# Optimization experiments

Measured on AMD Instinct MI355X. Metric: run time of the kernel, lower is better.

Reference implementation:

```python
import jax, jax.numpy as jnp
import numpy as np

DIM = 768
NUM_HEADS = 12
HEAD_DIM = DIM // NUM_HEADS
SCALE = HEAD_DIM ** -0.5


def setup_inputs() -> dict:
    key = jax.random.key(0)
    ks = jax.random.split(key, 7)
    B, N, C = 8, 1024, DIM
    x = jax.random.normal(ks[0], (B, N, C), dtype=jnp.float32)
    mask = jax.random.randint(ks[1], (B, N), 0, 2) > 0  # True = masked out
    qkv_w = jax.random.normal(ks[2], (3 * C, C), dtype=jnp.float32) * 0.02
    q_bias = jax.random.normal(ks[3], (C,), dtype=jnp.float32) * 0.02
    v_bias = jax.random.normal(ks[4], (C,), dtype=jnp.float32) * 0.02
    proj_w = jax.random.normal(ks[5], (C, C), dtype=jnp.float32) * 0.02
    proj_b = jax.random.normal(ks[6], (C,), dtype=jnp.float32) * 0.02
    return {"x": x, "mask": mask, "qkv_w": qkv_w, "q_bias": q_bias,
            "v_bias": v_bias, "proj_w": proj_w, "proj_b": proj_b}


def reference(x, mask, qkv_w, q_bias, v_bias, proj_w, proj_b):
    B, N, C = x.shape
    # CAE bias: concat(q_bias, zeros, v_bias) for the fused qkv projection
    qkv_bias = jnp.concatenate([q_bias, jnp.zeros_like(v_bias), v_bias])
    qkv = x @ qkv_w.T + qkv_bias  # [B, N, 3C]
    qkv = qkv.reshape(B, N, 3, NUM_HEADS, HEAD_DIM)
    q, k, v = (qkv[:, :, i].transpose(0, 2, 1, 3) for i in range(3))  # [B,H,N,hd]
    attn = jnp.einsum('bhqd,bhkd->bhqk', q * SCALE, k)  # [B,H,N,N]
    attn = jnp.where(mask[:, None, None, :], -jnp.inf, attn)
    attn = jax.nn.softmax(attn, axis=-1)
    out = jnp.einsum('bhqk,bhkd->bhqd', attn, v)  # [B,H,N,hd]
    out = out.transpose(0, 2, 1, 3).reshape(B, N, C)
    return out @ proj_w.T + proj_b
```

## Files before the change

### kernel.cpp

```cpp
#include <hip/hip_runtime.h>
#include <cstddef>
#include <cstdint>


typedef __attribute__((ext_vector_type(4))) float f32x4;
typedef __attribute__((ext_vector_type(8))) __bf16 bf16x8;
typedef __attribute__((ext_vector_type(4))) unsigned int uint4v;
typedef __attribute__((ext_vector_type(2))) unsigned int uint2v;

#define QK_PRESCALE 0.18033688011112042f

__device__ __forceinline__ unsigned short f2bf(float f) {
  return (unsigned short)((__float_as_uint(f) + 0x8000u) >> 16);
}
__device__ __forceinline__ unsigned int pack2bf(float flo, float fhi) {
  unsigned ulo = __float_as_uint(flo) + 0x8000u;
  unsigned uhi = __float_as_uint(fhi) + 0x8000u;
  return __builtin_amdgcn_perm(uhi, ulo, 0x07060302);
}

__device__ __forceinline__ void gl_lds16(const unsigned short* g, unsigned short* l) {
  __builtin_amdgcn_global_load_lds(
      (const __attribute__((address_space(1))) unsigned int*)g,
      (__attribute__((address_space(3))) unsigned int*)l, 16, 0, 0);
}

__global__ __launch_bounds__(256)
void cvt3_kernel(const float* __restrict__ s0, unsigned short* __restrict__ d0,
                 const float* __restrict__ s1, unsigned short* __restrict__ d1,
                 const float* __restrict__ s2, unsigned short* __restrict__ d2) {
  int bid = blockIdx.x;
  const float* s; unsigned short* d; int i; int n4;
  if (bid < 6144)      { s = s0; d = d0; i = bid * 256 + threadIdx.x;            n4 = 1572864; }
  else if (bid < 7872) { s = s1; d = d1; i = (bid - 6144) * 256 + threadIdx.x;   n4 = 442368; }
  else                 { s = s2; d = d2; i = (bid - 7872) * 256 + threadIdx.x;   n4 = 147456; }
  if (i < n4) {
    float4 v = ((const float4*)s)[i];
    uint2v o;
    o.x = pack2bf(v.x, v.y);
    o.y = pack2bf(v.z, v.w);
    ((uint2v*)d)[i] = o;
  }
}

__device__ __forceinline__ int a0row(int o) { return (o < 10) ? o * 8 : 144 + (o - 10) * 8; }
__device__ __forceinline__ int a1row(int o) { return (o < 8) ? 80 + o * 8 : 224 + (o - 8) * 8; }

__global__ __launch_bounds__(512, 2)
void qkv_gemm(const unsigned short* __restrict__ xb, const unsigned short* __restrict__ wb,
              const float* __restrict__ qb, const float* __restrict__ vb,
              unsigned short* __restrict__ qo, unsigned short* __restrict__ ko,
              unsigned short* __restrict__ vto) {
  __shared__ __align__(16) unsigned short lds[69632];
  const int tid = threadIdx.x;
  const int lane = tid & 63, wid = tid >> 6;
  const int widu = __builtin_amdgcn_readfirstlane(wid);
  const int lm = lane & 15, lq = lane >> 4;
  const int xsw = lm & 7;
  const int wr = widu >> 2, wc = widu & 3;
  const int L = blockIdx.x;
  const int xcd = L & 7, s = L >> 3;
  const int tt = xcd * 4 + (s >> 3);
  const int ft = s & 7;
  const int m0 = tt * 256;
  const int n0 = ft * 288;
  const int srow = lane >> 3;
  const int scolsw = ((lane & 7) ^ srow) * 8;
  const unsigned short* paS = wb + (size_t)(n0 + srow) * 768 + scolsw;
  const unsigned short* pbS = xb + (size_t)(m0 + srow) * 768 + scolsw;

  const int a0n3 = (widu < 4);
  const int a0o = a0n3 ? widu * 3 : 12 + (widu - 4) * 2;
  const int a0r0 = a0row(a0o), a0r1 = a0row(a0o + 1);
  const int a0r2 = a0n3 ? a0row(a0o + 2) : 0;
  const int a1r0 = a1row(2 * widu), a1r1 = a1row(2 * widu + 1);
  const int b0q0 = (2 * widu) >> 2, b0q1 = (2 * widu + 1) >> 2;
  const int b0r0 = b0q0 * 64 + ((2 * widu) & 3) * 8;
  const int b0r1 = b0q1 * 64 + ((2 * widu + 1) & 3) * 8;
  const int b1r0 = b0r0 + 32, b1r1 = b0r1 + 32;

  f32x4 acc[9][4] = {};

#define STAGE_A0(tgt) { const size_t _c = (size_t)(tgt) * 64; const int _b = ((tgt) & 1) * 18432; \
    gl_lds16(paS + (size_t)a0r0 * 768 + _c, &lds[_b + a0r0 * 64]); \
    gl_lds16(paS + (size_t)a0r1 * 768 + _c, &lds[_b + a0r1 * 64]); \
    if (a0n3) gl_lds16(paS + (size_t)a0r2 * 768 + _c, &lds[_b + a0r2 * 64]); }

#define STAGE_A1(tgt) { const size_t _c = (size_t)(tgt) * 64; const int _b = ((tgt) & 1) * 18432; \
    gl_lds16(paS + (size_t)a1r0 * 768 + _c, &lds[_b + a1r0 * 64]); \
    gl_lds16(paS + (size_t)a1r1 * 768 + _c, &lds[_b + a1r1 * 64]); }

#define STAGE_B0(tgt) { const size_t _c = (size_t)(tgt) * 64; const int _b = 36864 + ((tgt) & 1) * 16384; \
    gl_lds16(pbS + (size_t)b0r0 * 768 + _c, &lds[_b + b0r0 * 64]); \
    gl_lds16(pbS + (size_t)b0r1 * 768 + _c, &lds[_b + b0r1 * 64]); }

#define STAGE_B1(tgt) { const size_t _c = (size_t)(tgt) * 64; const int _b = 36864 + ((tgt) & 1) * 16384; \
    gl_lds16(pbS + (size_t)b1r0 * 768 + _c, &lds[_b + b1r0 * 64]); \
    gl_lds16(pbS + (size_t)b1r1 * 768 + _c, &lds[_b + b1r1 * 64]); }

#define WAIT_G() { if (a0n3) asm volatile("s_waitcnt vmcnt(5)" ::: "memory"); \
                   else      asm volatile("s_waitcnt vmcnt(4)" ::: "memory"); \
                   asm volatile("s_barrier" ::: "memory"); }
#define BAR_E()   asm volatile("s_waitcnt lgkmcnt(0)\ns_barrier" ::: "memory")

  STAGE_A0(0); STAGE_B0(0); STAGE_A1(0); STAGE_B1(0);
  STAGE_A0(1); STAGE_B0(1);
  WAIT_G();

  for (int t = 0; t < 12; ++t) {
    const int b = t & 1;
    const int tn1 = (t + 1 < 12) ? t + 1 : 11;
    const int tn2 = (t + 2 < 12) ? t + 2 : 11;
    const unsigned short* Ab = &lds[b * 18432];
    const unsigned short* Bb = &lds[36864 + b * 16384];

    bf16x8 bff[4][2], af[5][2];
#pragma unroll
    for (int n2 = 0; n2 < 4; ++n2)
#pragma unroll
      for (int kx = 0; kx < 2; ++kx)
        bff[n2][kx] = *(const bf16x8*)&Bb[(wc * 64 + n2 * 16 + lm) * 64 + (((kx * 4 + lq) ^ xsw) * 8)];
#pragma unroll
    for (int m2 = 0; m2 < 5; ++m2)
#pragma unroll
      for (int kx = 0; kx < 2; ++kx)
        af[m2][kx] = *(const bf16x8*)&Ab[(wr * 144 + m2 * 16 + lm) * 64 + (((kx * 4 + lq) ^ xsw) * 8)];

    STAGE_A1(tn1); STAGE_B1(tn1);

    __builtin_amdgcn_s_setprio(1);
#pragma unroll
    for (int kx = 0; kx < 2; ++kx)
#pragma unroll
      for (int m2 = 0; m2 < 5; ++m2)
#pragma unroll
        for (int n2 = 0; n2 < 4; ++n2)
          acc[m2][n2] = __builtin_amdgcn_mfma_f32_16x16x32_bf16(af[m2][kx], bff[n2][kx], acc[m2][n2], 0, 0, 0);
    __builtin_amdgcn_s_setprio(0);

    bf16x8 af2[4][2];
#pragma unroll
    for (int m2 = 0; m2 < 4; ++m2)
#pragma unroll
      for (int kx = 0; kx < 2; ++kx)
        af2[m2][kx] = *(const bf16x8*)&Ab[(wr * 144 + (5 + m2) * 16 + lm) * 64 + (((kx * 4 + lq) ^ xsw) * 8)];
    __builtin_amdgcn_s_setprio(1);
#pragma unroll
    for (int kx = 0; kx < 2; ++kx)
#pragma unroll
      for (int m2 = 0; m2 < 4; ++m2)
#pragma unroll
        for (int n2 = 0; n2 < 4; ++n2)
          acc[5 + m2][n2] = __builtin_amdgcn_mfma_f32_16x16x32_bf16(af2[m2][kx], bff[n2][kx], acc[5 + m2][n2], 0, 0, 0);
    __builtin_amdgcn_s_setprio(0);

    BAR_E();
    STAGE_A0(tn2); STAGE_B0(tn2);
    WAIT_G();
  }
  asm volatile("s_waitcnt vmcnt(0)" ::: "memory");

#undef STAGE_A0
#undef STAGE_A1
#undef STAGE_B0
#undef STAGE_B1

  const int bq = tt >> 2;
  const int tokb = (tt & 3) * 256;
#pragma unroll
  for (int mi = 0; mi < 9; ++mi) {
    const int fblk = n0 + wr * 144 + mi * 16;
    if (fblk < 1536) {
      const bool isq = fblk < 768;
      unsigned short* dst0 = isq ? qo : ko;
      const int fd = fblk - (isq ? 0 : 768);
      const int hh = fd >> 6;
      const int dih = (fd & 63) + lq * 4;
      f32x4 bias4 = {0.f, 0.f, 0.f, 0.f};
      if (isq) bias4 = *(const f32x4*)&qb[fblk + lq * 4];
#pragma unroll
      for (int ni = 0; ni < 4; ++ni) {
        const int tok = tokb + wc * 64 + ni * 16 + lm;
        uint2v pk;
        if (isq) {
          pk.x = pack2bf((acc[mi][ni][0] + bias4[0]) * QK_PRESCALE,
                         (acc[mi][ni][1] + bias4[1]) * QK_PRESCALE);
          pk.y = pack2bf((acc[mi][ni][2] + bias4[2]) * QK_PRESCALE,
                         (acc[mi][ni][3] + bias4[3]) * QK_PRESCALE);
        } else {
          pk.x = pack2bf(acc[mi][ni][0], acc[mi][ni][1]);
          pk.y = pack2bf(acc[mi][ni][2], acc[mi][ni][3]);
        }
        *(uint2v*)&dst0[(((size_t)(bq * 12 + hh)) * 1024 + tok) * 64 + dih] = pk;
      }
    }
  }
  if (n0 + 288 > 1536) {
#pragma unroll
    for (int p = 0; p < 2; ++p) {
      __syncthreads();
      if (wr == p) {
#pragma unroll
        for (int mi = 0; mi < 9; ++mi) {
          const int fblk = n0 + p * 144 + mi * 16;
          if (fblk >= 1536) {
            f32x4 bias4 = *(const f32x4*)&vb[fblk - 1536 + lq * 4];
#pragma unroll
            for (int ni = 0; ni < 4; ++ni) {
              const int tokl = wc * 64 + ni * 16 + lm;
#pragma unroll
              for (int r = 0; r < 4; ++r)
                lds[(mi * 16 + lq * 4 + r) * 264 + tokl] = f2bf(acc[mi][ni][r] + bias4[r]);
            }
          }
        }
      }
      __syncthreads();
      const int fv = 1536 - (n0 + p * 144);
      const int rv0 = fv > 0 ? fv : 0;
      for (int r = rv0 + (tid >> 2); r < 144; r += 128) {
        const int tq = tid & 3;
        const int dgv = n0 + p * 144 + r - 1536;
        const int hh = dgv >> 6, d = dgv & 63;
        unsigned short* dstv = vto + (((size_t)(bq * 12 + hh)) * 64 + d) * 1024 + tokb + tq * 64;
        const unsigned short* srcr = &lds[r * 264 + tq * 64];
#pragma unroll
        for (int j = 0; j < 8; ++j)
          *(uint4v*)&dstv[j * 8] = *(const uint4v*)&srcr[j * 8];
      }
    }
  }
}

__global__ __launch_bounds__(256)
void attn_mfma(const unsigned short* __restrict__ q, const unsigned short* __restrict__ k,
               const unsigned short* __restrict__ vt, const int* __restrict__ mask,
               unsigned short* __restrict__ ao) {
  __shared__ unsigned short ks_s[64 * 64];
  __shared__ unsigned short vs_s[64 * 64];
  __shared__ unsigned short ps[4][32 * 72];
  __shared__ float mkl[64];
  const int tid = threadIdx.x;
  const int lane = tid & 63, wid = tid >> 6;
  const int lm = lane & 15, lq = lane >> 4;
  const int xsw = lm & 7;
  const int L = blockIdx.x;
  const int xcd = L & 7, s = L >> 3;
  const int bh = xcd * 12 + s / 8;
  const int qt = s % 8;
  const int bb = bh / 12, hh = bh % 12;
  const unsigned short* qp = q + (size_t)bh * 65536;
  const unsigned short* kp = k + (size_t)bh * 65536;
  const unsigned short* vp = vt + (size_t)bh * 65536;
  const int* mp = mask + bb * 1024;
  const int q0 = qt * 128 + wid * 32;
  const int srow = lane >> 3;
  const int scolsw = ((lane & 7) ^ srow) * 8;
  const unsigned short* gk = kp + (size_t)(wid * 16 + srow) * 64 + scolsw;
  const unsigned short* gv = vp + (size_t)(wid * 16 + srow) * 1024 + scolsw;

  bf16x8 qf[2][2];
#pragma unroll
  for (int mi = 0; mi < 2; ++mi)
#pragma unroll
    for (int ks2 = 0; ks2 < 2; ++ks2)
      qf[mi][ks2] = *(const bf16x8*)&qp[(size_t)(q0 + mi * 16 + lm) * 64 + ks2 * 32 + lq * 8];
  bf16x8 ones;
#pragma unroll
  for (int i = 0; i < 8; ++i) ones[i] = (__bf16)1.0f;

  f32x4 o_acc[2][4] = {};
  f32x4 l_acc[2] = {};

  for (int kt = 0; kt < 16; ++kt) {
    __syncthreads();
#pragma unroll
    for (int i = 0; i < 2; ++i) {
      gl_lds16(gk + (size_t)kt * 4096 + (size_t)i * 8 * 64, &ks_s[(wid * 16 + i * 8) * 64]);
      gl_lds16(gv + (size_t)kt * 64 + (size_t)i * 8 * 1024, &vs_s[(wid * 16 + i * 8) * 64]);
    }
    if (tid < 64) mkl[tid] = mp[kt * 64 + tid] ? -1e30f : 0.0f;
    __syncthreads();

    f32x4 st[4][2] = {};
#pragma unroll
    for (int ks2 = 0; ks2 < 2; ++ks2) {
      bf16x8 kf[4];
#pragma unroll
      for (int nt = 0; nt < 4; ++nt)
        kf[nt] = *(const bf16x8*)&ks_s[(nt * 16 + lm) * 64 + (((ks2 * 4 + lq) ^ xsw) * 8)];
#pragma unroll
      for (int nt = 0; nt < 4; ++nt)
#pragma unroll
        for (int mi = 0; mi < 2; ++mi)
          st[nt][mi] = __builtin_amdgcn_mfma_f32_16x16x32_bf16(kf[nt], qf[mi][ks2], st[nt][mi], 0, 0, 0);
    }

#pragma unroll
    for (int nt = 0; nt < 4; ++nt) {
      f32x4 mv4 = *(const f32x4*)&mkl[nt * 16 + lq * 4];
#pragma unroll
      for (int mi = 0; mi < 2; ++mi) {
        uint2v pk;
        pk.x = pack2bf(__builtin_amdgcn_exp2f(st[nt][mi][0] + mv4[0]),
                       __builtin_amdgcn_exp2f(st[nt][mi][1] + mv4[1]));
        pk.y = pack2bf(__builtin_amdgcn_exp2f(st[nt][mi][2] + mv4[2]),
                       __builtin_amdgcn_exp2f(st[nt][mi][3] + mv4[3]));
        *(uint2v*)&ps[wid][(mi * 16 + lm) * 72 + nt * 16 + lq * 4] = pk;
      }
    }

#pragma unroll
    for (int ks2 = 0; ks2 < 2; ++ks2) {
      bf16x8 pf[2], vf[4];
#pragma unroll
      for (int mi = 0; mi < 2; ++mi)
        pf[mi] = *(const bf16x8*)&ps[wid][(mi * 16 + lm) * 72 + ks2 * 32 + lq * 8];
#pragma unroll
      for (int nt = 0; nt < 4; ++nt)
        vf[nt] = *(const bf16x8*)&vs_s[(nt * 16 + lm) * 64 + (((ks2 * 4 + lq) ^ xsw) * 8)];
#pragma unroll
      for (int mi = 0; mi < 2; ++mi) {
#pragma unroll
        for (int nt = 0; nt < 4; ++nt)
          o_acc[mi][nt] = __builtin_amdgcn_mfma_f32_16x16x32_bf16(pf[mi], vf[nt], o_acc[mi][nt], 0, 0, 0);
        l_acc[mi] = __builtin_amdgcn_mfma_f32_16x16x32_bf16(pf[mi], ones, l_acc[mi], 0, 0, 0);
      }
    }
  }

#pragma unroll
  for (int mi = 0; mi < 2; ++mi) {
#pragma unroll
    for (int r = 0; r < 4; ++r) {
      float inv = 1.0f / l_acc[mi][r];
      int tok = q0 + mi * 16 + lq * 4 + r;
#pragma unroll
      for (int nt = 0; nt < 4; ++nt)
        ao[(size_t)(bb * 1024 + tok) * 768 + hh * 64 + nt * 16 + lm] = f2bf(o_acc[mi][nt][r] * inv);
    }
  }
}

__global__ __launch_bounds__(256)
void proj_gemm(const unsigned short* __restrict__ ab, const unsigned short* __restrict__ wb,
               const float* __restrict__ pb, float* __restrict__ out) {
  __shared__ unsigned short as[128 * 64];
  __shared__ unsigned short bs[128 * 64];
  const int tid = threadIdx.x;
  const int lane = tid & 63, wid = tid >> 6;
  const int lm = lane & 15, lq = lane >> 4;
  const int xsw = lm & 7;
  const int wm = (wid & 1) * 64, wn = (wid >> 1) * 64;
  const int L = blockIdx.x;
  const int xcd = L & 7, s = L >> 3;
  const int m0 = (xcd * 8 + s / 6) * 128;
  const int n0 = (s % 6) * 128;
  const int srow = lane >> 3;
  const int scolsw = ((lane & 7) ^ srow) * 8;
  const unsigned short* ga = wb + (size_t)(n0 + wid * 32 + srow) * 768 + scolsw;
  const unsigned short* gb = ab + (size_t)(m0 + wid * 32 + srow) * 768 + scolsw;
  f32x4 acc[4][4] = {};
  for (int kt = 0; kt < 768; kt += 64) {
#pragma unroll
    for (int i = 0; i < 4; ++i) {
      gl_lds16(ga + kt + (size_t)i * 8 * 768, &as[(wid * 32 + i * 8) * 64]);
      gl_lds16(gb + kt + (size_t)i * 8 * 768, &bs[(wid * 32 + i * 8) * 64]);
    }
    __syncthreads();
#pragma unroll
    for (int ks = 0; ks < 2; ++ks) {
      bf16x8 af[4], bf[4];
#pragma unroll
      for (int i = 0; i < 4; ++i)
        af[i] = *(const bf16x8*)&as[(wm + i * 16 + lm) * 64 + (((ks * 4 + lq) ^ xsw) * 8)];
#pragma unroll
      for (int i = 0; i < 4; ++i)
        bf[i] = *(const bf16x8*)&bs[(wn + i * 16 + lm) * 64 + (((ks * 4 + lq) ^ xsw) * 8)];
#pragma unroll
      for (int mi = 0; mi < 4; ++mi)
#pragma unroll
        for (int ni = 0; ni < 4; ++ni)
          acc[mi][ni] = __builtin_amdgcn_mfma_f32_16x16x32_bf16(af[mi], bf[ni], acc[mi][ni], 0, 0, 0);
    }
    __syncthreads();
  }
#pragma unroll
  for (int mi = 0; mi < 4; ++mi) {
    int gn0 = n0 + wm + mi * 16 + lq * 4;
    f32x4 bias4 = *(const f32x4*)&pb[gn0];
#pragma unroll
    for (int ni = 0; ni < 4; ++ni) {
      int gm = m0 + wn + ni * 16 + lm;
      f32x4 o;
      o[0] = acc[mi][ni][0] + bias4[0];
      o[1] = acc[mi][ni][1] + bias4[1];
      o[2] = acc[mi][ni][2] + bias4[2];
      o[3] = acc[mi][ni][3] + bias4[3];
      *(f32x4*)&out[(size_t)gm * 768 + gn0] = o;
    }
  }
}

extern "C" void kernel_launch(void* const* d_in, const int* in_sizes, int n_in,
                              void* d_out, int out_size, void* d_ws, size_t ws_size,
                              hipStream_t stream) {
  const float* x      = (const float*)d_in[0];
  const int*   mask   = (const int*)d_in[1];
  const float* qkv_w  = (const float*)d_in[2];
  const float* q_bias = (const float*)d_in[3];
  const float* v_bias = (const float*)d_in[4];
  const float* proj_w = (const float*)d_in[5];
  const float* proj_b = (const float*)d_in[6];
  float* out = (float*)d_out;
  unsigned short* p = (unsigned short*)d_ws;
  unsigned short* xb     = p;              p += 6291456;
  unsigned short* wqkvb  = p;              p += 1769472;
  unsigned short* wprojb = p;              p += 589824;
  unsigned short* qo     = p;              p += 6291456;
  unsigned short* ko     = p;              p += 6291456;
  unsigned short* vto    = p;              p += 6291456;
  unsigned short* ao     = p;

  cvt3_kernel<<<8448, 256, 0, stream>>>(x, xb, qkv_w, wqkvb, proj_w, wprojb);
  qkv_gemm<<<256, 512, 0, stream>>>(xb, wqkvb, q_bias, v_bias, qo, ko, vto);
  attn_mfma<<<768, 256, 0, stream>>>(qo, ko, vto, mask, ao);
  proj_gemm<<<384, 256, 0, stream>>>(ao, wprojb, proj_b, out);
}
```

Before: 183.1 us.

## Double-buffer K/V tiles in attention and interleave softmax with PV MFMA

The attention kernel now double-buffers K and V tiles in LDS, prefetching tile kt+1 while computing on tile kt, so one barrier per iteration replaces two. The whole mask row is converted to float bias once up front instead of per tile. The P scratch buffer shrinks to a half-tile with an XOR swizzle, and exp/pack is interleaved with the PV MFMAs in two halves. s_setprio hints and a launch-bounds occupancy target of 3 are added, which trades more LDS per block and register pressure for overlap of global loads with compute.

```diff
diff --git a/kernel.cpp b/kernel.cpp
--- a/kernel.cpp
+++ b/kernel.cpp
@@ -232,18 +232,19 @@
   }
 }
 
-__global__ __launch_bounds__(256)
+__global__ __launch_bounds__(256, 3)
 void attn_mfma(const unsigned short* __restrict__ q, const unsigned short* __restrict__ k,
                const unsigned short* __restrict__ vt, const int* __restrict__ mask,
                unsigned short* __restrict__ ao) {
-  __shared__ unsigned short ks_s[64 * 64];
-  __shared__ unsigned short vs_s[64 * 64];
-  __shared__ unsigned short ps[4][32 * 72];
-  __shared__ float mkl[64];
+  __shared__ unsigned short ks_s[2][64 * 64];
+  __shared__ unsigned short vs_s[2][64 * 64];
+  __shared__ unsigned short ps[4][32 * 40];
+  __shared__ float mkl[1024];
   const int tid = threadIdx.x;
   const int lane = tid & 63, wid = tid >> 6;
   const int lm = lane & 15, lq = lane >> 4;
   const int xsw = lm & 7;
+  const int sxor = (lm & 8) >> 1;
   const int L = blockIdx.x;
   const int xcd = L & 7, s = L >> 3;
   const int bh = xcd * 12 + s / 8;
@@ -259,6 +260,22 @@
   const unsigned short* gk = kp + (size_t)(wid * 16 + srow) * 64 + scolsw;
   const unsigned short* gv = vp + (size_t)(wid * 16 + srow) * 1024 + scolsw;
 
+#define STAGE_T(kt_, b_) { \
+    gl_lds16(gk + (size_t)(kt_) * 4096, &ks_s[b_][(wid * 16) * 64]); \
+    gl_lds16(gk + (size_t)(kt_) * 4096 + (size_t)8 * 64, &ks_s[b_][(wid * 16 + 8) * 64]); \
+    gl_lds16(gv + (size_t)(kt_) * 64, &vs_s[b_][(wid * 16) * 64]); \
+    gl_lds16(gv + (size_t)(kt_) * 64 + (size_t)8 * 1024, &vs_s[b_][(wid * 16 + 8) * 64]); }
+
+  {
+    int4 mv = ((const int4*)mp)[tid];
+    float4 f;
+    f.x = mv.x ? -1e30f : 0.0f;
+    f.y = mv.y ? -1e30f : 0.0f;
+    f.z = mv.z ? -1e30f : 0.0f;
+    f.w = mv.w ? -1e30f : 0.0f;
+    ((float4*)mkl)[tid] = f;
+  }
+
   bf16x8 qf[2][2];
 #pragma unroll
   for (int mi = 0; mi < 2; ++mi)
@@ -272,15 +289,15 @@
   f32x4 o_acc[2][4] = {};
   f32x4 l_acc[2] = {};
 
+  STAGE_T(0, 0);
+  __syncthreads();
+
   for (int kt = 0; kt < 16; ++kt) {
-    __syncthreads();
-#pragma unroll
-    for (int i = 0; i < 2; ++i) {
-      gl_lds16(gk + (size_t)kt * 4096 + (size_t)i * 8 * 64, &ks_s[(wid * 16 + i * 8) * 64]);
-      gl_lds16(gv + (size_t)kt * 64 + (size_t)i * 8 * 1024, &vs_s[(wid * 16 + i * 8) * 64]);
-    }
-    if (tid < 64) mkl[tid] = mp[kt * 64 + tid] ? -1e30f : 0.0f;
-    __syncthreads();
+    const int b = kt & 1;
+    if (kt) {
+      asm volatile("s_waitcnt vmcnt(0)\ns_barrier" ::: "memory");
+    }
+    if (kt < 15) STAGE_T(kt + 1, b ^ 1);
 
     f32x4 st[4][2] = {};
 #pragma unroll
@@ -288,37 +305,44 @@
       bf16x8 kf[4];
 #pragma unroll
       for (int nt = 0; nt < 4; ++nt)
-        kf[nt] = *(const bf16x8*)&ks_s[(nt * 16 + lm) * 64 + (((ks2 * 4 + lq) ^ xsw) * 8)];
+        kf[nt] = *(const bf16x8*)&ks_s[b][(nt * 16 + lm) * 64 + (((ks2 * 4 + lq) ^ xsw) * 8)];
+      __builtin_amdgcn_s_setprio(1);
 #pragma unroll
       for (int nt = 0; nt < 4; ++nt)
 #pragma unroll
         for (int mi = 0; mi < 2; ++mi)
           st[nt][mi] = __builtin_amdgcn_mfma_f32_16x16x32_bf16(kf[nt], qf[mi][ks2], st[nt][mi], 0, 0, 0);
-    }
-
-#pragma unroll
-    for (int nt = 0; nt < 4; ++nt) {
-      f32x4 mv4 = *(const f32x4*)&mkl[nt * 16 + lq * 4];
+      __builtin_amdgcn_s_setprio(0);
+    }
+
+#pragma unroll
+    for (int h2 = 0; h2 < 2; ++h2) {
+#pragma unroll
+      for (int ntl = 0; ntl < 2; ++ntl) {
+        const int nt = h2 * 2 + ntl;
+        f32x4 mv4 = *(const f32x4*)&mkl[kt * 64 + nt * 16 + lq * 4];
+#pragma unroll
+        for (int mi = 0; mi < 2; ++mi) {
+          uint2v pk;
+          pk.x = pack2bf(__builtin_amdgcn_exp2f(st[nt][mi][0] + mv4[0]),
+                         __builtin_amdgcn_exp2f(st[nt][mi][1] + mv4[1]));
+          pk.y = pack2bf(__builtin_amdgcn_exp2f(st[nt][mi][2] + mv4[2]),
+                         __builtin_amdgcn_exp2f(st[nt][mi][3] + mv4[3]));
+          *(uint2v*)&ps[wid][(mi * 16 + lm) * 40 + ((ntl * 16 + lq * 4) ^ sxor)] = pk;
+        }
+      }
+      bf16x8 pf[2], vf[4];
 #pragma unroll
       for (int mi = 0; mi < 2; ++mi) {
-        uint2v pk;
-        pk.x = pack2bf(__builtin_amdgcn_exp2f(st[nt][mi][0] + mv4[0]),
-                       __builtin_amdgcn_exp2f(st[nt][mi][1] + mv4[1]));
-        pk.y = pack2bf(__builtin_amdgcn_exp2f(st[nt][mi][2] + mv4[2]),
-                       __builtin_amdgcn_exp2f(st[nt][mi][3] + mv4[3]));
-        *(uint2v*)&ps[wid][(mi * 16 + lm) * 72 + nt * 16 + lq * 4] = pk;
-      }
-    }
-
-#pragma unroll
-    for (int ks2 = 0; ks2 < 2; ++ks2) {
-      bf16x8 pf[2], vf[4];
-#pragma unroll
-      for (int mi = 0; mi < 2; ++mi)
-        pf[mi] = *(const bf16x8*)&ps[wid][(mi * 16 + lm) * 72 + ks2 * 32 + lq * 8];
+        uint2v h0 = *(const uint2v*)&ps[wid][(mi * 16 + lm) * 40 + ((lq * 8) ^ sxor)];
+        uint2v h1 = *(const uint2v*)&ps[wid][(mi * 16 + lm) * 40 + ((lq * 8 + 4) ^ sxor)];
+        uint4v u; u.x = h0.x; u.y = h0.y; u.z = h1.x; u.w = h1.y;
+        pf[mi] = __builtin_bit_cast(bf16x8, u);
+      }
 #pragma unroll
       for (int nt = 0; nt < 4; ++nt)
-        vf[nt] = *(const bf16x8*)&vs_s[(nt * 16 + lm) * 64 + (((ks2 * 4 + lq) ^ xsw) * 8)];
+        vf[nt] = *(const bf16x8*)&vs_s[b][(nt * 16 + lm) * 64 + (((h2 * 4 + lq) ^ xsw) * 8)];
+      __builtin_amdgcn_s_setprio(1);
 #pragma unroll
       for (int mi = 0; mi < 2; ++mi) {
 #pragma unroll
@@ -326,8 +350,10 @@
           o_acc[mi][nt] = __builtin_amdgcn_mfma_f32_16x16x32_bf16(pf[mi], vf[nt], o_acc[mi][nt], 0, 0, 0);
         l_acc[mi] = __builtin_amdgcn_mfma_f32_16x16x32_bf16(pf[mi], ones, l_acc[mi], 0, 0, 0);
       }
-    }
-  }
+      __builtin_amdgcn_s_setprio(0);
+    }
+  }
+#undef STAGE_T
 
 #pragma unroll
   for (int mi = 0; mi < 2; ++mi) {
```

Result: no change. 182.1 us (-0.5%).
